# Optimization experiments

Hardware: AMD Instinct MI355X
Metric: run time of the kernel (lower is better)

Reference implementation:

```python
import jax, jax.numpy as jnp
import numpy as np

UNITS, D_IN, K_CONN, BATCH = 1024, 2048, 16, 4096
TEMP = 1.0  # temperature_update_tf at step=0 (epoch 0)
EPS = 1e-20


def setup_inputs() -> dict:
    key = jax.random.key(0)
    kx, kw, kd, kg = jax.random.split(key, 4)
    x = jax.random.normal(kx, (BATCH, D_IN), dtype=jnp.float32)
    # he_uniform for W
    limit = np.sqrt(6.0 / D_IN).astype(np.float32)
    W = jax.random.uniform(kw, (UNITS, D_IN), minval=-limit, maxval=limit, dtype=jnp.float32)
    # logits D ~ N(0, 0.5)
    D = 0.5 * jax.random.normal(kd, (UNITS, D_IN), dtype=jnp.float32)
    # Gumbel noise, scaled by -0.001 as in the original (BS=1)
    u = jax.random.uniform(kg, (1, UNITS, D_IN), dtype=jnp.float32)
    GN = -0.001 * jnp.log(-jnp.log(u + EPS) + EPS)
    return {"x": x, "W": W, "D": D, "GN": GN, "k": K_CONN}


def _hard_sigmoid(v):
    return jnp.clip(0.2 * v + 0.5, 0.0, 1.0)


def reference(x, W, D, GN, k):
    logits = D  # [units, d]
    perturbed = logits[None, :, :] + GN  # [1, units, d]
    # top-k indices, then sorted ascending (TF: top_k of indices + reverse)
    _, idx = jax.lax.top_k(perturbed, k)           # [1, units, k]
    idx_sorted = jnp.sort(idx, axis=-1)             # ascending index order
    hard = jax.nn.one_hot(idx_sorted, D_IN, dtype=perturbed.dtype)  # [1, units, k, d]
    # exclusive cumsum over the k axis
    cum = jnp.cumsum(hard, axis=-2) - hard
    # softmax((log(exp(logits)*(1-cum+eps)) + GN)/Temp) == softmax((logits + log(1-cum+eps) + GN)/Temp)
    scores = (logits[None, :, None, :] + jnp.log(1.0 - cum + EPS) + GN[:, :, None, :]) / TEMP
    soft = jax.nn.softmax(scores, axis=-1)          # [1, units, k, d]
    samples = jax.lax.stop_gradient(hard - soft) + soft
    A = samples.sum(axis=-2).sum(axis=0)            # [units, d]
    # straight-through binary weights
    w_soft = 2.0 * _hard_sigmoid(W) - 1.0
    w_bin = jax.lax.stop_gradient(jnp.sign(W) - w_soft) + w_soft
    AW = A * w_bin                                   # [units, d]
    y = x @ AW.T                                     # [batch, units]
    return y
```

## Files before the change

kernel.cpp:

```cpp
#include <hip/hip_runtime.h>
#include <hip/hip_bf16.h>

#define UNITS 1024
#define DIN   2048
#define KCONN 16
#define BATCH 4096
#define BB    8

typedef float    f32x4 __attribute__((ext_vector_type(4)));
typedef unsigned u32x4 __attribute__((ext_vector_type(4)));
typedef int      i32x4 __attribute__((ext_vector_type(4)));

#define LDNT4F(P) __builtin_nontemporal_load((const f32x4*)(P))

__global__ __launch_bounds__(256) void topk_sel_kernel(
    const float* __restrict__ Dl, const float* __restrict__ GN,
    const float* __restrict__ W, int* __restrict__ selP) {
  const int lane = threadIdx.x & 63;
  const int wv   = threadIdx.x >> 6;
  const int u    = blockIdx.x * 4 + wv;

  const f32x4* D4 = (const f32x4*)(Dl + (size_t)u * DIN);
  const f32x4* G4 = (const f32x4*)(GN + (size_t)u * DIN);
  float v[32];
#pragma unroll
  for (int i4 = 0; i4 < 8; ++i4) {
    f32x4 d = LDNT4F(D4 + i4 * 64 + lane);
    f32x4 g = LDNT4F(G4 + i4 * 64 + lane);
    v[i4 * 4 + 0] = d[0] + g[0];
    v[i4 * 4 + 1] = d[1] + g[1];
    v[i4 * 4 + 2] = d[2] + g[2];
    v[i4 * 4 + 3] = d[3] + g[3];
  }

  float m1 = -INFINITY, m2 = -INFINITY;
  int   l1 = 0, l2 = 0;
#pragma unroll
  for (int l = 0; l < 32; ++l) {
    float xv = v[l];
    bool g1t = xv > m1;
    bool g2t = xv > m2;
    m2 = g1t ? m1 : (g2t ? xv : m2);
    l2 = g1t ? l1 : (g2t ? l : l2);
    m1 = g1t ? xv : m1;
    l1 = g1t ? l  : l1;
  }

  unsigned claimed = 0;
  int navail = 2;
  int gsel = 0;

#pragma unroll 1
  for (int it = 0; it < KCONN; ++it) {
    unsigned kb = __float_as_uint(m1);
    unsigned kv = kb ^ (((int)kb < 0) ? 0xFFFFFFFFu : 0x80000000u);
    int g1 = ((l1 >> 2) << 8) | (lane << 2) | (l1 & 3);
    unsigned rk = kv; int rg = g1;
#define DSTEP(CTRL, RM) { \
    unsigned k2_ = (unsigned)__builtin_amdgcn_update_dpp((int)rk, (int)rk, CTRL, RM, 0xF, false); \
    int g2_ = __builtin_amdgcn_update_dpp(rg, rg, CTRL, RM, 0xF, false); \
    bool tk_ = (k2_ > rk) || ((k2_ == rk) && (g2_ < rg)); \
    rk = tk_ ? k2_ : rk; rg = tk_ ? g2_ : rg; }
    DSTEP(0x111, 0xF)
    DSTEP(0x112, 0xF)
    DSTEP(0x114, 0xF)
    DSTEP(0x118, 0xF)
    DSTEP(0x142, 0xA)
    DSTEP(0x143, 0xC)
#undef DSTEP
    int wg = __builtin_amdgcn_readlane(rg, 63);
    if (lane == it) gsel = wg;

    bool own  = (g1 == wg);
    bool need = own && (navail == 1);
    if (own) claimed |= 1u << l1;
    if (own && navail == 2) { m1 = m2; l1 = l2; navail = 1; }
    if (need) {
      float bm = -INFINITY; int bl = 0;
#pragma unroll
      for (int l = 0; l < 32; ++l) {
        float xv = (claimed & (1u << l)) ? -INFINITY : v[l];
        if (xv > bm) { bm = xv; bl = l; }
      }
      m1 = bm; l1 = bl;
    }
  }

  if (lane < KCONN) {
    int g = gsel;
    float w = W[(size_t)u * DIN + g];
    int sd = g ^ ((g >> 3) & 7);
    int pa = (w == 0.0f) ? (DIN << 1)
                         : ((sd << 1) | (w < 0.0f ? 1 : 0));
    selP[u * KCONN + lane] = pa;
  }
}

__global__ __launch_bounds__(512) void gather_mm_kernel(
    const float* __restrict__ x, const int* __restrict__ selP,
    float* __restrict__ y) {
  __shared__ u32x4 xs[DIN + 1];
  const int t = threadIdx.x;
  const size_t b0 = (size_t)blockIdx.x * BB;

  const i32x4* S0 = (const i32x4*)(selP + t * KCONN);
  const i32x4* S1 = (const i32x4*)(selP + (t + 512) * KCONN);
  i32x4 sA0 = S0[0], sA1 = S0[1], sA2 = S0[2], sA3 = S0[3];
  i32x4 sB0 = S1[0], sB1 = S1[1], sB2 = S1[2], sB3 = S1[3];

  const float* xb = x + b0 * DIN + 4 * t;
  f32x4 r0 = LDNT4F(xb + 0 * DIN);
  f32x4 r1 = LDNT4F(xb + 1 * DIN);
  f32x4 r2 = LDNT4F(xb + 2 * DIN);
  f32x4 r3 = LDNT4F(xb + 3 * DIN);
  f32x4 r4 = LDNT4F(xb + 4 * DIN);
  f32x4 r5 = LDNT4F(xb + 5 * DIN);
  f32x4 r6 = LDNT4F(xb + 6 * DIN);
  f32x4 r7 = LDNT4F(xb + 7 * DIN);

#define PK2(LO, HI) ({ __hip_bfloat16 l_ = __float2bfloat16(LO), h_ = __float2bfloat16(HI); \
  (unsigned)(*(unsigned short*)&l_) | ((unsigned)(*(unsigned short*)&h_) << 16); })
#pragma unroll
  for (int j = 0; j < 4; ++j) {
    const int d  = 4 * t + j;
    const int sd = d ^ ((d >> 3) & 7);
    u32x4 ch;
    ch[0] = PK2(r0[j], r1[j]);
    ch[1] = PK2(r2[j], r3[j]);
    ch[2] = PK2(r4[j], r5[j]);
    ch[3] = PK2(r6[j], r7[j]);
    xs[sd] = ch;
  }
#undef PK2
  if (t == 0) { u32x4 z = {0, 0, 0, 0}; xs[DIN] = z; }
  __syncthreads();

#define GJ(PA) { unsigned pa_ = (unsigned)(PA); \
  u32x4 vv_ = xs[pa_ >> 1]; \
  unsigned sm_ = (pa_ & 1u) ? 0x80008000u : 0u; \
  vv_[0] ^= sm_; vv_[1] ^= sm_; vv_[2] ^= sm_; vv_[3] ^= sm_; \
  a0 += __uint_as_float(vv_[0] << 16); a1 += __uint_as_float(vv_[0] & 0xffff0000u); \
  a2 += __uint_as_float(vv_[1] << 16); a3 += __uint_as_float(vv_[1] & 0xffff0000u); \
  a4 += __uint_as_float(vv_[2] << 16); a5 += __uint_as_float(vv_[2] & 0xffff0000u); \
  a6 += __uint_as_float(vv_[3] << 16); a7 += __uint_as_float(vv_[3] & 0xffff0000u); }

#define UNIT(SA, SB, SC, SD, U) { \
  float a0 = 0, a1 = 0, a2 = 0, a3 = 0, a4 = 0, a5 = 0, a6 = 0, a7 = 0; \
  GJ(SA[0]) GJ(SA[1]) GJ(SA[2]) GJ(SA[3]) \
  GJ(SB[0]) GJ(SB[1]) GJ(SB[2]) GJ(SB[3]) \
  GJ(SC[0]) GJ(SC[1]) GJ(SC[2]) GJ(SC[3]) \
  GJ(SD[0]) GJ(SD[1]) GJ(SD[2]) GJ(SD[3]) \
  const int u_ = (U); \
  __builtin_nontemporal_store(a0, &y[(b0 + 0) * UNITS + u_]); \
  __builtin_nontemporal_store(a1, &y[(b0 + 1) * UNITS + u_]); \
  __builtin_nontemporal_store(a2, &y[(b0 + 2) * UNITS + u_]); \
  __builtin_nontemporal_store(a3, &y[(b0 + 3) * UNITS + u_]); \
  __builtin_nontemporal_store(a4, &y[(b0 + 4) * UNITS + u_]); \
  __builtin_nontemporal_store(a5, &y[(b0 + 5) * UNITS + u_]); \
  __builtin_nontemporal_store(a6, &y[(b0 + 6) * UNITS + u_]); \
  __builtin_nontemporal_store(a7, &y[(b0 + 7) * UNITS + u_]); }

  UNIT(sA0, sA1, sA2, sA3, t)
  UNIT(sB0, sB1, sB2, sB3, t + 512)
#undef UNIT
#undef GJ
}

extern "C" void kernel_launch(void* const* d_in, const int* in_sizes, int n_in,
                              void* d_out, int out_size, void* d_ws, size_t ws_size,
                              hipStream_t stream) {
  const float* x  = (const float*)d_in[0];
  const float* W  = (const float*)d_in[1];
  const float* Dl = (const float*)d_in[2];
  const float* GN = (const float*)d_in[3];
  float* y = (float*)d_out;

  int* selP = (int*)d_ws;

  topk_sel_kernel<<<UNITS / 4, 256, 0, stream>>>(Dl, GN, W, selP);
  gather_mm_kernel<<<BATCH / BB, 512, 0, stream>>>(x, selP, y);
}
```

Baseline: 26.50 us.

## Fuse top-k selection and gather matmul into one kernel with grid barrier

Merges the top-k selection kernel and the gather/matmul kernel into a single 512-block launch. Two waves per block compute the selections for two units while the block streams its x rows into registers, and a software grid-wide barrier (an atomic counter in the workspace) separates the phases. The intent is to remove the inter-kernel gap and overlap the x loads with the selection work. In exchange it adds a memset launch, spin-wait overhead, and relies on all 512 blocks being co-resident to avoid deadlock.

```diff
diff --git a/kernel.cpp b/kernel.cpp
--- a/kernel.cpp
+++ b/kernel.cpp
@@ -6,6 +6,7 @@
 #define KCONN 16
 #define BATCH 4096
 #define BB    8
+#define NBLK  512
 
 typedef float    f32x4 __attribute__((ext_vector_type(4)));
 typedef unsigned u32x4 __attribute__((ext_vector_type(4)));
@@ -13,100 +14,94 @@
 
 #define LDNT4F(P) __builtin_nontemporal_load((const f32x4*)(P))
 
-__global__ __launch_bounds__(256) void topk_sel_kernel(
+__global__ __launch_bounds__(512, 4) void fused_kernel(
+    const float* __restrict__ x, const float* __restrict__ W,
     const float* __restrict__ Dl, const float* __restrict__ GN,
-    const float* __restrict__ W, int* __restrict__ selP) {
-  const int lane = threadIdx.x & 63;
-  const int wv   = threadIdx.x >> 6;
-  const int u    = blockIdx.x * 4 + wv;
+    unsigned* __restrict__ bar, int* __restrict__ selP,
+    float* __restrict__ y) {
+  __shared__ u32x4 xs[DIN + 1];
+  const int t    = threadIdx.x;
+  const int wave = t >> 6;
+  const int lane = t & 63;
+  const size_t b0 = (size_t)blockIdx.x * BB;
 
-  const f32x4* D4 = (const f32x4*)(Dl + (size_t)u * DIN);
-  const f32x4* G4 = (const f32x4*)(GN + (size_t)u * DIN);
-  float v[32];
+  if (wave < 2) {
+    const int u = blockIdx.x * 2 + wave;
+    const f32x4* D4 = (const f32x4*)(Dl + (size_t)u * DIN);
+    const f32x4* G4 = (const f32x4*)(GN + (size_t)u * DIN);
+    float v[32];
 #pragma unroll
-  for (int i4 = 0; i4 < 8; ++i4) {
-    f32x4 d = LDNT4F(D4 + i4 * 64 + lane);
-    f32x4 g = LDNT4F(G4 + i4 * 64 + lane);
-    v[i4 * 4 + 0] = d[0] + g[0];
-    v[i4 * 4 + 1] = d[1] + g[1];
-    v[i4 * 4 + 2] = d[2] + g[2];
-    v[i4 * 4 + 3] = d[3] + g[3];
-  }
+    for (int i4 = 0; i4 < 8; ++i4) {
+      f32x4 d = LDNT4F(D4 + i4 * 64 + lane);
+      f32x4 g = LDNT4F(G4 + i4 * 64 + lane);
+      v[i4 * 4 + 0] = d[0] + g[0];
+      v[i4 * 4 + 1] = d[1] + g[1];
+      v[i4 * 4 + 2] = d[2] + g[2];
+      v[i4 * 4 + 3] = d[3] + g[3];
+    }
 
-  float m1 = -INFINITY, m2 = -INFINITY;
-  int   l1 = 0, l2 = 0;
+    float m1 = -INFINITY, m2 = -INFINITY;
+    int   l1 = 0, l2 = 0;
 #pragma unroll
-  for (int l = 0; l < 32; ++l) {
-    float xv = v[l];
-    bool g1t = xv > m1;
-    bool g2t = xv > m2;
-    m2 = g1t ? m1 : (g2t ? xv : m2);
-    l2 = g1t ? l1 : (g2t ? l : l2);
-    m1 = g1t ? xv : m1;
-    l1 = g1t ? l  : l1;
-  }
+    for (int l = 0; l < 32; ++l) {
+      float xv = v[l];
+      bool g1t = xv > m1;
+      bool g2t = xv > m2;
+      m2 = g1t ? m1 : (g2t ? xv : m2);
+      l2 = g1t ? l1 : (g2t ? l : l2);
+      m1 = g1t ? xv : m1;
+      l1 = g1t ? l  : l1;
+    }
 
-  unsigned claimed = 0;
-  int navail = 2;
-  int gsel = 0;
+    unsigned claimed = 0;
+    int navail = 2;
+    int gsel = 0;
 
 #pragma unroll 1
-  for (int it = 0; it < KCONN; ++it) {
-    unsigned kb = __float_as_uint(m1);
-    unsigned kv = kb ^ (((int)kb < 0) ? 0xFFFFFFFFu : 0x80000000u);
-    int g1 = ((l1 >> 2) << 8) | (lane << 2) | (l1 & 3);
-    unsigned rk = kv; int rg = g1;
+    for (int it = 0; it < KCONN; ++it) {
+      unsigned kb = __float_as_uint(m1);
+      unsigned kv = kb ^ (((int)kb < 0) ? 0xFFFFFFFFu : 0x80000000u);
+      int g1 = ((l1 >> 2) << 8) | (lane << 2) | (l1 & 3);
+      unsigned rk = kv; int rg = g1;
 #define DSTEP(CTRL, RM) { \
-    unsigned k2_ = (unsigned)__builtin_amdgcn_update_dpp((int)rk, (int)rk, CTRL, RM, 0xF, false); \
-    int g2_ = __builtin_amdgcn_update_dpp(rg, rg, CTRL, RM, 0xF, false); \
-    bool tk_ = (k2_ > rk) || ((k2_ == rk) && (g2_ < rg)); \
-    rk = tk_ ? k2_ : rk; rg = tk_ ? g2_ : rg; }
-    DSTEP(0x111, 0xF)
-    DSTEP(0x112, 0xF)
-    DSTEP(0x114, 0xF)
-    DSTEP(0x118, 0xF)
-    DSTEP(0x142, 0xA)
-    DSTEP(0x143, 0xC)
+      unsigned k2_ = (unsigned)__builtin_amdgcn_update_dpp((int)rk, (int)rk, CTRL, RM, 0xF, false); \
+      int g2_ = __builtin_amdgcn_update_dpp(rg, rg, CTRL, RM, 0xF, false); \
+      bool tk_ = (k2_ > rk) || ((k2_ == rk) && (g2_ < rg)); \
+      rk = tk_ ? k2_ : rk; rg = tk_ ? g2_ : rg; }
+      DSTEP(0x111, 0xF)
+      DSTEP(0x112, 0xF)
+      DSTEP(0x114, 0xF)
+      DSTEP(0x118, 0xF)
+      DSTEP(0x142, 0xA)
+      DSTEP(0x143, 0xC)
 #undef DSTEP
-    int wg = __builtin_amdgcn_readlane(rg, 63);
-    if (lane == it) gsel = wg;
+      int wg = __builtin_amdgcn_readlane(rg, 63);
+      if (lane == it) gsel = wg;
 
-    bool own  = (g1 == wg);
-    bool need = own && (navail == 1);
-    if (own) claimed |= 1u << l1;
-    if (own && navail == 2) { m1 = m2; l1 = l2; navail = 1; }
-    if (need) {
-      float bm = -INFINITY; int bl = 0;
+      bool own  = (g1 == wg);
+      bool need = own && (navail == 1);
+      if (own) claimed |= 1u << l1;
+      if (own && navail == 2) { m1 = m2; l1 = l2; navail = 1; }
+      if (need) {
+        float bm = -INFINITY; int bl = 0;
 #pragma unroll
-      for (int l = 0; l < 32; ++l) {
-        float xv = (claimed & (1u << l)) ? -INFINITY : v[l];
-        if (xv > bm) { bm = xv; bl = l; }
+        for (int l = 0; l < 32; ++l) {
+          float xv = (claimed & (1u << l)) ? -INFINITY : v[l];
+          if (xv > bm) { bm = xv; bl = l; }
+        }
+        m1 = bm; l1 = bl;
       }
-      m1 = bm; l1 = bl;
+    }
+
+    if (lane < KCONN) {
+      int g = gsel;
+      float w = W[(size_t)u * DIN + g];
+      int sd = g ^ ((g >> 3) & 7);
+      int pa = (w == 0.0f) ? (DIN << 1)
+                           : ((sd << 1) | (w < 0.0f ? 1 : 0));
+      selP[u * KCONN + lane] = pa;
     }
   }
-
-  if (lane < KCONN) {
-    int g = gsel;
-    float w = W[(size_t)u * DIN + g];
-    int sd = g ^ ((g >> 3) & 7);
-    int pa = (w == 0.0f) ? (DIN << 1)
-                         : ((sd << 1) | (w < 0.0f ? 1 : 0));
-    selP[u * KCONN + lane] = pa;
-  }
-}
-
-__global__ __launch_bounds__(512) void gather_mm_kernel(
-    const float* __restrict__ x, const int* __restrict__ selP,
-    float* __restrict__ y) {
-  __shared__ u32x4 xs[DIN + 1];
-  const int t = threadIdx.x;
-  const size_t b0 = (size_t)blockIdx.x * BB;
-
-  const i32x4* S0 = (const i32x4*)(selP + t * KCONN);
-  const i32x4* S1 = (const i32x4*)(selP + (t + 512) * KCONN);
-  i32x4 sA0 = S0[0], sA1 = S0[1], sA2 = S0[2], sA3 = S0[3];
-  i32x4 sB0 = S1[0], sB1 = S1[1], sB2 = S1[2], sB3 = S1[3];
 
   const float* xb = x + b0 * DIN + 4 * t;
   f32x4 r0 = LDNT4F(xb + 0 * DIN);
@@ -117,6 +112,26 @@
   f32x4 r5 = LDNT4F(xb + 5 * DIN);
   f32x4 r6 = LDNT4F(xb + 6 * DIN);
   f32x4 r7 = LDNT4F(xb + 7 * DIN);
+
+  __syncthreads();
+  if (t == 0) {
+    unsigned old = __hip_atomic_fetch_add(bar, 1u, __ATOMIC_ACQ_REL,
+                                          __HIP_MEMORY_SCOPE_AGENT);
+    if (old == NBLK - 1) {
+      __hip_atomic_store(bar, 0u, __ATOMIC_RELEASE, __HIP_MEMORY_SCOPE_AGENT);
+    } else {
+      while (__hip_atomic_load(bar, __ATOMIC_ACQUIRE,
+                               __HIP_MEMORY_SCOPE_AGENT) != 0u) {
+        __builtin_amdgcn_s_sleep(1);
+      }
+    }
+  }
+  __syncthreads();
+
+  const i32x4* S0 = (const i32x4*)(selP + t * KCONN);
+  const i32x4* S1 = (const i32x4*)(selP + (t + 512) * KCONN);
+  i32x4 sA0 = S0[0], sA1 = S0[1], sA2 = S0[2], sA3 = S0[3];
+  i32x4 sB0 = S1[0], sB1 = S1[1], sB2 = S1[2], sB3 = S1[3];
 
 #define PK2(LO, HI) ({ __hip_bfloat16 l_ = __float2bfloat16(LO), h_ = __float2bfloat16(HI); \
   (unsigned)(*(unsigned short*)&l_) | ((unsigned)(*(unsigned short*)&h_) << 16); })
@@ -175,8 +190,9 @@
   const float* GN = (const float*)d_in[3];
   float* y = (float*)d_out;
 
-  int* selP = (int*)d_ws;
+  unsigned* bar  = (unsigned*)d_ws;
+  int*      selP = (int*)((char*)d_ws + 128);
 
-  topk_sel_kernel<<<UNITS / 4, 256, 0, stream>>>(Dl, GN, W, selP);
-  gather_mm_kernel<<<BATCH / BB, 512, 0, stream>>>(x, selP, y);
+  hipMemsetAsync(d_ws, 0, 128, stream);
+  fused_kernel<<<NBLK, 512, 0, stream>>>(x, W, Dl, GN, bar, selP, y);
 }
```

New measurement: 84.29 us. +218.1%, slower.
